# Performance work log

Hardware: AMD Instinct MI355X
Metric: run time of the kernel (lower is better)

## Reference

```python
import jax, jax.numpy as jnp
import numpy as np

# Dims: N tokens, D input, H expert hidden, O output, E experts, G gate hidden, K top-k
N, D, H, O, E, G, K = 8192, 1024, 2048, 1024, 8, 256, 2
BALANCE_COEF = 0.01


def setup_inputs() -> dict:
    key = jax.random.key(0)
    ks = jax.random.split(key, 12)
    def lin(k, shape, fan_in):
        return jax.random.normal(k, shape, jnp.float32) * (1.0 / np.sqrt(fan_in))
    return {
        "x":   jax.random.normal(ks[0], (N, D), jnp.float32),
        # gating MLP: D -> G -> E
        "Wg1": lin(ks[1], (D, G), D), "bg1": jnp.zeros((G,), jnp.float32),
        "Wg2": lin(ks[2], (G, E), G), "bg2": jnp.zeros((E,), jnp.float32),
        # stacked expert MLPs: D -> H -> H -> O (ExpertNetwork, num_layers=2)
        "W1": lin(ks[3], (E, D, H), D), "b1": jnp.zeros((E, H), jnp.float32),
        "W2": lin(ks[4], (E, H, H), H), "b2": jnp.zeros((E, H), jnp.float32),
        "W3": lin(ks[5], (E, H, O), H), "b3": jnp.zeros((E, O), jnp.float32),
    }


def reference(x, Wg1, bg1, Wg2, bg2, W1, b1, W2, b2, W3, b3):
    # Gating: 2-layer MLP -> softmax -> top-k -> renormalize (eval: no noise/dropout)
    logits = jnp.maximum(x @ Wg1 + bg1, 0.0) @ Wg2 + bg2            # [N, E]
    probs = jax.nn.softmax(logits, axis=-1)
    w, idx = jax.lax.top_k(probs, K)                                # [N, K]
    w = w / jnp.sum(w, axis=-1, keepdims=True)
    onehot = jax.nn.one_hot(idx, E, dtype=x.dtype)                  # [N, K, E]
    comb = jnp.sum(onehot * w[..., None], axis=1)                   # [N, E] per-token expert weight

    # Dense-equivalent combine: unselected tokens get weight 0, identical math to
    # the masked dispatch + scatter-add in the torch code.
    def expert_step(acc, params):
        W1e, b1e, W2e, b2e, W3e, b3e, we = params                   # we: [N]
        h = jnp.maximum(x @ W1e + b1e, 0.0)                         # [N, H]
        h = jnp.maximum(h @ W2e + b2e, 0.0)                         # [N, H]
        o = h @ W3e + b3e                                           # [N, O]
        return acc + o * we[:, None], None

    out, _ = jax.lax.scan(expert_step, jnp.zeros((N, O), x.dtype),
                          (W1, b1, W2, b2, W3, b3, comb.T))

    # aux losses: expert_usage[e] = sum_i mean_b(indices[b,i]==e)
    expert_usage = jnp.sum(onehot, axis=(0, 1)) / N                 # [E]
    balance_loss = jnp.mean((expert_usage - 1.0 / E) ** 2) * BALANCE_COEF
    return out, balance_loss, expert_usage
```

## Files before the change

### kernel.cpp

```cpp
#include <hip/hip_runtime.h>
#include <hip/hip_bf16.h>
#include <cstdint>
#include <cstddef>

#define N_TOK 8192
#define D_IN  1024
#define H_DIM 2048
#define O_DIM 1024
#define E_NUM 8
#define G_DIM 256
#define MAXTILES 136
#define MAXROWS  (MAXTILES*128)

typedef __attribute__((ext_vector_type(8))) __bf16 bf16x8;
typedef __attribute__((ext_vector_type(4))) __bf16 bf16x4;
typedef __attribute__((ext_vector_type(4))) float floatx4;

#define GCAST(p) ((__attribute__((address_space(1))) void*)(void*)(p))
#define LCAST(p) ((__attribute__((address_space(3))) void*)(p))

__global__ __launch_bounds__(256) void cast_x_kernel(const float* __restrict__ x,
                                                     __bf16* __restrict__ xb) {
  int i = (blockIdx.x * 256 + threadIdx.x) * 4;
  float4 v = *reinterpret_cast<const float4*>(x + i);
  bf16x4 o;
  o.x = (__bf16)v.x; o.y = (__bf16)v.y; o.z = (__bf16)v.z; o.w = (__bf16)v.w;
  *reinterpret_cast<bf16x4*>(xb + i) = o;
}

__global__ __launch_bounds__(256) void transpose_w_kernel(const float* __restrict__ src,
                                                          __bf16* __restrict__ dst,
                                                          int K, int N) {
  __shared__ float tl[32][33];
  int e = blockIdx.z;
  const float* s = src + (size_t)e * K * N;
  __bf16* d = dst + (size_t)e * K * N;
  int k0 = blockIdx.y * 32, n0 = blockIdx.x * 32;
  int t = threadIdx.x;
  int r = t >> 5, c = t & 31;
#pragma unroll
  for (int i = 0; i < 4; i++)
    tl[r + i * 8][c] = s[(size_t)(k0 + r + i * 8) * N + n0 + c];
  __syncthreads();
#pragma unroll
  for (int i = 0; i < 4; i++)
    d[(size_t)(n0 + r + i * 8) * K + k0 + c] = (__bf16)tl[c][r + i * 8];
}

__global__ __launch_bounds__(256) void gate1_kernel(const float* __restrict__ x,
                                                    const float* __restrict__ Wg1,
                                                    const float* __restrict__ bg1,
                                                    float* __restrict__ g) {
  __shared__ float As[32][68];
  __shared__ float Bs[32][68];
  int bn = blockIdx.x, bm = blockIdx.y;
  int t = threadIdx.x;
  int tm = t >> 4, tn = t & 15;
  float acc[4][4] = {};
  for (int k0 = 0; k0 < D_IN; k0 += 32) {
#pragma unroll
    for (int i = 0; i < 2; i++) {
      int idx = t + 256 * i;
      int row = idx >> 3, c4 = idx & 7;
      float4 v = *reinterpret_cast<const float4*>(
          x + (size_t)(bm * 64 + row) * D_IN + k0 + c4 * 4);
      As[c4 * 4 + 0][row] = v.x;
      As[c4 * 4 + 1][row] = v.y;
      As[c4 * 4 + 2][row] = v.z;
      As[c4 * 4 + 3][row] = v.w;
      int brow = idx >> 4, bc4 = idx & 15;
      float4 wv = *reinterpret_cast<const float4*>(
          Wg1 + (size_t)(k0 + brow) * G_DIM + bn * 64 + bc4 * 4);
      *reinterpret_cast<float4*>(&Bs[brow][bc4 * 4]) = wv;
    }
    __syncthreads();
#pragma unroll
    for (int k = 0; k < 32; k++) {
      float4 av = *reinterpret_cast<const float4*>(&As[k][tm * 4]);
      float4 bv = *reinterpret_cast<const float4*>(&Bs[k][tn * 4]);
      float a4[4] = {av.x, av.y, av.z, av.w};
      float b4[4] = {bv.x, bv.y, bv.z, bv.w};
#pragma unroll
      for (int r = 0; r < 4; r++)
#pragma unroll
        for (int c = 0; c < 4; c++) acc[r][c] = fmaf(a4[r], b4[c], acc[r][c]);
    }
    __syncthreads();
  }
  int gr = bm * 64 + tm * 4, gc = bn * 64 + tn * 4;
#pragma unroll
  for (int r = 0; r < 4; r++) {
    float4 o;
    o.x = fmaxf(acc[r][0] + bg1[gc + 0], 0.f);
    o.y = fmaxf(acc[r][1] + bg1[gc + 1], 0.f);
    o.z = fmaxf(acc[r][2] + bg1[gc + 2], 0.f);
    o.w = fmaxf(acc[r][3] + bg1[gc + 3], 0.f);
    *reinterpret_cast<float4*>(g + (size_t)(gr + r) * G_DIM + gc) = o;
  }
}

__global__ __launch_bounds__(256) void gate2_kernel(const float* __restrict__ g,
                                                    const float* __restrict__ Wg2,
                                                    const float* __restrict__ bg2,
                                                    int* __restrict__ top_idx,
                                                    float* __restrict__ top_w,
                                                    int* __restrict__ counts) {
  __shared__ float lg[32][9];
  int t = threadIdx.x;
  int tl = t >> 3, e = t & 7;
  int n = blockIdx.x * 32 + tl;
  const float* gr = g + (size_t)n * G_DIM;
  float acc = bg2[e];
  for (int i = 0; i < G_DIM; i += 4) {
    float4 v = *reinterpret_cast<const float4*>(gr + i);
    acc += v.x * Wg2[(i + 0) * E_NUM + e];
    acc += v.y * Wg2[(i + 1) * E_NUM + e];
    acc += v.z * Wg2[(i + 2) * E_NUM + e];
    acc += v.w * Wg2[(i + 3) * E_NUM + e];
  }
  lg[tl][e] = acc;
  __syncthreads();
  if (e == 0) {
    float l[8];
#pragma unroll
    for (int i = 0; i < 8; i++) l[i] = lg[tl][i];
    int i0 = 0;
    for (int i = 1; i < 8; i++)
      if (l[i] > l[i0]) i0 = i;
    int i1 = (i0 == 0) ? 1 : 0;
    for (int i = 0; i < 8; i++)
      if (i != i0 && l[i] > l[i1]) i1 = i;
    float d = expf(l[i1] - l[i0]);
    float w0 = 1.f / (1.f + d);
    float w1 = d * w0;
    top_idx[n * 2 + 0] = i0;
    top_idx[n * 2 + 1] = i1;
    top_w[n * 2 + 0] = w0;
    top_w[n * 2 + 1] = w1;
    atomicAdd(&counts[i0], 1);
    atomicAdd(&counts[i1], 1);
  }
}

__global__ void g3_kernel(const int* __restrict__ counts, int* __restrict__ cursors,
                          int* __restrict__ off_pad, int* __restrict__ ntiles,
                          int* __restrict__ tile_meta, float* __restrict__ out_tail) {
  if (threadIdx.x == 0) {
    int off = 0, nt = 0;
    float mse = 0.f;
    for (int e = 0; e < E_NUM; e++) {
      off_pad[e] = off;
      int c = counts[e];
      int tiles = (c + 127) >> 7;
      for (int i = 0; i < tiles; i++) {
        tile_meta[nt * 2 + 0] = e;
        tile_meta[nt * 2 + 1] = off + i * 128;
        nt++;
      }
      off += tiles << 7;
      cursors[e] = 0;
      float u = (float)c / (float)N_TOK;
      out_tail[1 + e] = u;
      float dd = u - 0.125f;
      mse += dd * dd;
    }
    *ntiles = nt;
    out_tail[0] = (mse / 8.0f) * 0.01f;
  }
}

__global__ __launch_bounds__(256) void init_rows_kernel(int* __restrict__ slot_token,
                                                        float* __restrict__ slot_w) {
  int s = blockIdx.x * 256 + threadIdx.x;
  slot_token[s] = 0;
  slot_w[s] = 0.f;
}

__global__ __launch_bounds__(256) void scatter_kernel(const int* __restrict__ top_idx,
                                                      const float* __restrict__ top_w,
                                                      const int* __restrict__ off_pad,
                                                      int* __restrict__ cursors,
                                                      int* __restrict__ slot_token,
                                                      float* __restrict__ slot_w) {
  int n = blockIdx.x * 256 + threadIdx.x;
#pragma unroll
  for (int k = 0; k < 2; k++) {
    int e = top_idx[n * 2 + k];
    int pos = atomicAdd(&cursors[e], 1);
    int s = off_pad[e] + pos;
    slot_token[s] = n;
    slot_w[s] = top_w[n * 2 + k];
  }
}

__global__ __launch_bounds__(256) void moe_gemm_kernel(
    const __bf16* __restrict__ A, int Astride, int gatherA,
    const __bf16* __restrict__ Wt, const float* __restrict__ bias,
    int Kdim, int Ndim,
    const int* __restrict__ tile_meta, const int* __restrict__ ntiles_p,
    const int* __restrict__ slot_token, const float* __restrict__ slot_w,
    __bf16* __restrict__ h_out, float* __restrict__ out_final, int finalMode) {
  int tile = blockIdx.y;
  if (tile >= *ntiles_p) return;
  __shared__ __bf16 As[128 * 32];
  __shared__ __bf16 Bs[128 * 32];
  int ex = tile_meta[tile * 2 + 0];
  int slot0 = tile_meta[tile * 2 + 1];
  int n0 = blockIdx.x * 128;
  int t = threadIdx.x, l = t & 63, w = t >> 6;

  size_t aoff[2], boff[2];
#pragma unroll
  for (int i = 0; i < 2; i++) {
    int gidx = (w * 2 + i) * 64 + l;
    int row = gidx >> 2, kch = gidx & 3;
    int sl = slot0 + row;
    long long rb = gatherA ? (long long)slot_token[sl] * Astride
                           : (long long)sl * Astride;
    aoff[i] = (size_t)rb + kch * 8;
    boff[i] = ((size_t)ex * Ndim + n0 + row) * (size_t)Kdim + kch * 8;
  }

  int wm = (w >> 1) * 64, wn = (w & 1) * 64;
  int lm = l & 15, lq = l >> 4;
  floatx4 acc[4][4] = {};

  for (int k0 = 0; k0 < Kdim; k0 += 32) {
#pragma unroll
    for (int i = 0; i < 2; i++) {
      __builtin_amdgcn_global_load_lds(GCAST(A + aoff[i] + k0),
                                       LCAST((char*)As + w * 2048 + i * 1024),
                                       16, 0, 0);
      __builtin_amdgcn_global_load_lds(GCAST(Wt + boff[i] + k0),
                                       LCAST((char*)Bs + w * 2048 + i * 1024),
                                       16, 0, 0);
    }
    __syncthreads();
    bf16x8 af[4], bfr[4];
#pragma unroll
    for (int i = 0; i < 4; i++)
      af[i] = *reinterpret_cast<const bf16x8*>(As + (wm + i * 16 + lm) * 32 + lq * 8);
#pragma unroll
    for (int j = 0; j < 4; j++)
      bfr[j] = *reinterpret_cast<const bf16x8*>(Bs + (wn + j * 16 + lm) * 32 + lq * 8);
#pragma unroll
    for (int i = 0; i < 4; i++)
#pragma unroll
      for (int j = 0; j < 4; j++)
        acc[i][j] = __builtin_amdgcn_mfma_f32_16x16x32_bf16(af[i], bfr[j], acc[i][j], 0, 0, 0);
    __syncthreads();
  }

  float bcol[4];
#pragma unroll
  for (int j = 0; j < 4; j++) bcol[j] = bias[(size_t)ex * Ndim + n0 + wn + j * 16 + lm];

  if (finalMode) {
#pragma unroll
    for (int i = 0; i < 4; i++) {
#pragma unroll
      for (int r = 0; r < 4; r++) {
        int sl = slot0 + wm + i * 16 + lq * 4 + r;
        int tok = slot_token[sl];
        float wgt = slot_w[sl];
        float* orow = out_final + (size_t)tok * Ndim + n0 + wn + lm;
#pragma unroll
        for (int j = 0; j < 4; j++) {
          float v = acc[i][j][r] + bcol[j];
          atomicAdd(orow + j * 16, wgt * v);
        }
      }
    }
  } else {
#pragma unroll
    for (int i = 0; i < 4; i++) {
#pragma unroll
      for (int r = 0; r < 4; r++) {
        int sl = slot0 + wm + i * 16 + lq * 4 + r;
        __bf16* hrow = h_out + (size_t)sl * Ndim + n0 + wn + lm;
#pragma unroll
        for (int j = 0; j < 4; j++) {
          float v = fmaxf(acc[i][j][r] + bcol[j], 0.f);
          hrow[j * 16] = (__bf16)v;
        }
      }
    }
  }
}

extern "C" void kernel_launch(void* const* d_in, const int* in_sizes, int n_in,
                              void* d_out, int out_size, void* d_ws, size_t ws_size,
                              hipStream_t stream) {
  const float* x   = (const float*)d_in[0];
  const float* Wg1 = (const float*)d_in[1];
  const float* bg1 = (const float*)d_in[2];
  const float* Wg2 = (const float*)d_in[3];
  const float* bg2 = (const float*)d_in[4];
  const float* W1  = (const float*)d_in[5];
  const float* b1  = (const float*)d_in[6];
  const float* W2  = (const float*)d_in[7];
  const float* b2  = (const float*)d_in[8];
  const float* W3  = (const float*)d_in[9];
  const float* b3  = (const float*)d_in[10];
  float* out = (float*)d_out;

  char* ws = (char*)d_ws;
  __bf16* x_bf       = (__bf16*)(ws + 0);
  __bf16* W1t        = (__bf16*)(ws + 16777216);
  __bf16* W2t        = (__bf16*)(ws + 50331648);
  __bf16* W3t        = (__bf16*)(ws + 117440512);
  __bf16* h1         = (__bf16*)(ws + 150994944);
  __bf16* h2         = (__bf16*)(ws + 222298112);
  float*  gbuf       = (float*) (ws + 293601280);
  int*    top_idx    = (int*)   (ws + 301989888);
  float*  top_w      = (float*) (ws + 302055424);
  int*    slot_token = (int*)   (ws + 302120960);
  float*  slot_w     = (float*) (ws + 302190592);
  int*    meta       = (int*)   (ws + 302260224);
  int* counts    = meta;
  int* cursors   = meta + 8;
  int* off_pad   = meta + 16;
  int* ntiles    = meta + 24;
  int* tile_meta = meta + 32;
  float* out_tail = out + (size_t)N_TOK * O_DIM;

  hipMemsetAsync(d_out, 0, ((size_t)N_TOK * O_DIM + 9) * sizeof(float), stream);
  hipMemsetAsync(meta, 0, 64, stream);

  cast_x_kernel<<<(N_TOK * D_IN) / 1024, 256, 0, stream>>>(x, x_bf);
  transpose_w_kernel<<<dim3(H_DIM / 32, D_IN / 32, E_NUM), 256, 0, stream>>>(W1, W1t, D_IN, H_DIM);
  transpose_w_kernel<<<dim3(H_DIM / 32, H_DIM / 32, E_NUM), 256, 0, stream>>>(W2, W2t, H_DIM, H_DIM);
  transpose_w_kernel<<<dim3(O_DIM / 32, H_DIM / 32, E_NUM), 256, 0, stream>>>(W3, W3t, H_DIM, O_DIM);

  gate1_kernel<<<dim3(G_DIM / 64, N_TOK / 64), 256, 0, stream>>>(x, Wg1, bg1, gbuf);
  gate2_kernel<<<N_TOK / 32, 256, 0, stream>>>(gbuf, Wg2, bg2, top_idx, top_w, counts);
  g3_kernel<<<1, 64, 0, stream>>>(counts, cursors, off_pad, ntiles, tile_meta, out_tail);
  init_rows_kernel<<<MAXROWS / 256, 256, 0, stream>>>(slot_token, slot_w);
  scatter_kernel<<<N_TOK / 256, 256, 0, stream>>>(top_idx, top_w, off_pad, cursors,
                                                  slot_token, slot_w);

  moe_gemm_kernel<<<dim3(H_DIM / 128, MAXTILES), 256, 0, stream>>>(
      x_bf, D_IN, 1, W1t, b1, D_IN, H_DIM, tile_meta, ntiles, slot_token, slot_w,
      h1, nullptr, 0);
  moe_gemm_kernel<<<dim3(H_DIM / 128, MAXTILES), 256, 0, stream>>>(
      h1, H_DIM, 0, W2t, b2, H_DIM, H_DIM, tile_meta, ntiles, slot_token, slot_w,
      h2, nullptr, 0);
  moe_gemm_kernel<<<dim3(O_DIM / 128, MAXTILES), 256, 0, stream>>>(
      h2, H_DIM, 0, W3t, b3, H_DIM, O_DIM, tile_meta, ntiles, slot_token, slot_w,
      nullptr, out, 1);
}
```

Measured before the change: 1.148 ms.

## Swizzle GEMM LDS tiles, widen weight transpose, fuse slot init, skip padded atomics

Applies an XOR swizzle to the k-chunk placement in the MoE GEMM's LDS tiles so the MFMA fragment reads hit fewer bank conflicts. Rewrites the weight transpose to use 64x64 tiles with float4 loads and 16-byte bf16 stores. Folds the slot_token/slot_w zeroing into g3_kernel, which removes one launch but does the zeroing in a single block. Also skips the output atomicAdds for padded rows whose weight is zero.

```diff
diff --git a/kernel.cpp b/kernel.cpp
--- a/kernel.cpp
+++ b/kernel.cpp
@@ -31,20 +31,28 @@
 __global__ __launch_bounds__(256) void transpose_w_kernel(const float* __restrict__ src,
                                                           __bf16* __restrict__ dst,
                                                           int K, int N) {
-  __shared__ float tl[32][33];
+  __shared__ float tl[64][68];
   int e = blockIdx.z;
   const float* s = src + (size_t)e * K * N;
   __bf16* d = dst + (size_t)e * K * N;
-  int k0 = blockIdx.y * 32, n0 = blockIdx.x * 32;
+  int k0 = blockIdx.y * 64, n0 = blockIdx.x * 64;
   int t = threadIdx.x;
-  int r = t >> 5, c = t & 31;
-#pragma unroll
-  for (int i = 0; i < 4; i++)
-    tl[r + i * 8][c] = s[(size_t)(k0 + r + i * 8) * N + n0 + c];
+  int kr = t >> 4, nc = t & 15;
+#pragma unroll
+  for (int p = 0; p < 4; p++) {
+    float4 v = *reinterpret_cast<const float4*>(
+        s + (size_t)(k0 + kr + p * 16) * N + n0 + nc * 4);
+    *reinterpret_cast<float4*>(&tl[kr + p * 16][nc * 4]) = v;
+  }
   __syncthreads();
-#pragma unroll
-  for (int i = 0; i < 4; i++)
-    d[(size_t)(n0 + r + i * 8) * K + k0 + c] = (__bf16)tl[c][r + i * 8];
+  int n = t >> 2, kg = t & 3;
+#pragma unroll
+  for (int p = 0; p < 2; p++) {
+    bf16x8 o;
+#pragma unroll
+    for (int j = 0; j < 8; j++) o[j] = (__bf16)tl[p * 32 + kg * 8 + j][n];
+    *reinterpret_cast<bf16x8*>(d + (size_t)(n0 + n) * K + k0 + p * 32 + kg * 8) = o;
+  }
 }
 
 __global__ __launch_bounds__(256) void gate1_kernel(const float* __restrict__ x,
@@ -144,7 +152,8 @@
 
 __global__ void g3_kernel(const int* __restrict__ counts, int* __restrict__ cursors,
                           int* __restrict__ off_pad, int* __restrict__ ntiles,
-                          int* __restrict__ tile_meta, float* __restrict__ out_tail) {
+                          int* __restrict__ tile_meta, float* __restrict__ out_tail,
+                          int* __restrict__ slot_token, float* __restrict__ slot_w) {
   if (threadIdx.x == 0) {
     int off = 0, nt = 0;
     float mse = 0.f;
@@ -167,13 +176,10 @@
     *ntiles = nt;
     out_tail[0] = (mse / 8.0f) * 0.01f;
   }
-}
-
-__global__ __launch_bounds__(256) void init_rows_kernel(int* __restrict__ slot_token,
-                                                        float* __restrict__ slot_w) {
-  int s = blockIdx.x * 256 + threadIdx.x;
-  slot_token[s] = 0;
-  slot_w[s] = 0.f;
+  for (int s = threadIdx.x; s < MAXROWS; s += 256) {
+    slot_token[s] = 0;
+    slot_w[s] = 0.f;
+  }
 }
 
 __global__ __launch_bounds__(256) void scatter_kernel(const int* __restrict__ top_idx,
@@ -213,7 +219,8 @@
 #pragma unroll
   for (int i = 0; i < 2; i++) {
     int gidx = (w * 2 + i) * 64 + l;
-    int row = gidx >> 2, kch = gidx & 3;
+    int row = gidx >> 2;
+    int kch = (gidx & 3) ^ ((row >> 1) & 3);
     int sl = slot0 + row;
     long long rb = gatherA ? (long long)slot_token[sl] * Astride
                            : (long long)sl * Astride;
@@ -238,11 +245,17 @@
     __syncthreads();
     bf16x8 af[4], bfr[4];
 #pragma unroll
-    for (int i = 0; i < 4; i++)
-      af[i] = *reinterpret_cast<const bf16x8*>(As + (wm + i * 16 + lm) * 32 + lq * 8);
-#pragma unroll
-    for (int j = 0; j < 4; j++)
-      bfr[j] = *reinterpret_cast<const bf16x8*>(Bs + (wn + j * 16 + lm) * 32 + lq * 8);
+    for (int i = 0; i < 4; i++) {
+      int r = wm + i * 16 + lm;
+      int s = lq ^ ((r >> 1) & 3);
+      af[i] = *reinterpret_cast<const bf16x8*>(As + r * 32 + s * 8);
+    }
+#pragma unroll
+    for (int j = 0; j < 4; j++) {
+      int r = wn + j * 16 + lm;
+      int s = lq ^ ((r >> 1) & 3);
+      bfr[j] = *reinterpret_cast<const bf16x8*>(Bs + r * 32 + s * 8);
+    }
 #pragma unroll
     for (int i = 0; i < 4; i++)
 #pragma unroll
@@ -263,11 +276,13 @@
         int sl = slot0 + wm + i * 16 + lq * 4 + r;
         int tok = slot_token[sl];
         float wgt = slot_w[sl];
-        float* orow = out_final + (size_t)tok * Ndim + n0 + wn + lm;
-#pragma unroll
-        for (int j = 0; j < 4; j++) {
-          float v = acc[i][j][r] + bcol[j];
-          atomicAdd(orow + j * 16, wgt * v);
+        if (wgt != 0.f) {
+          float* orow = out_final + (size_t)tok * Ndim + n0 + wn + lm;
+#pragma unroll
+          for (int j = 0; j < 4; j++) {
+            float v = acc[i][j][r] + bcol[j];
+            atomicAdd(orow + j * 16, wgt * v);
+          }
         }
       }
     }
@@ -328,14 +343,14 @@
   hipMemsetAsync(meta, 0, 64, stream);
 
   cast_x_kernel<<<(N_TOK * D_IN) / 1024, 256, 0, stream>>>(x, x_bf);
-  transpose_w_kernel<<<dim3(H_DIM / 32, D_IN / 32, E_NUM), 256, 0, stream>>>(W1, W1t, D_IN, H_DIM);
-  transpose_w_kernel<<<dim3(H_DIM / 32, H_DIM / 32, E_NUM), 256, 0, stream>>>(W2, W2t, H_DIM, H_DIM);
-  transpose_w_kernel<<<dim3(O_DIM / 32, H_DIM / 32, E_NUM), 256, 0, stream>>>(W3, W3t, H_DIM, O_DIM);
+  transpose_w_kernel<<<dim3(H_DIM / 64, D_IN / 64, E_NUM), 256, 0, stream>>>(W1, W1t, D_IN, H_DIM);
+  transpose_w_kernel<<<dim3(H_DIM / 64, H_DIM / 64, E_NUM), 256, 0, stream>>>(W2, W2t, H_DIM, H_DIM);
+  transpose_w_kernel<<<dim3(O_DIM / 64, H_DIM / 64, E_NUM), 256, 0, stream>>>(W3, W3t, H_DIM, O_DIM);
 
   gate1_kernel<<<dim3(G_DIM / 64, N_TOK / 64), 256, 0, stream>>>(x, Wg1, bg1, gbuf);
   gate2_kernel<<<N_TOK / 32, 256, 0, stream>>>(gbuf, Wg2, bg2, top_idx, top_w, counts);
-  g3_kernel<<<1, 64, 0, stream>>>(counts, cursors, off_pad, ntiles, tile_meta, out_tail);
-  init_rows_kernel<<<MAXROWS / 256, 256, 0, stream>>>(slot_token, slot_w);
+  g3_kernel<<<1, 256, 0, stream>>>(counts, cursors, off_pad, ntiles, tile_meta, out_tail,
+                                   slot_token, slot_w);
   scatter_kernel<<<N_TOK / 256, 256, 0, stream>>>(top_idx, top_w, off_pad, cursors,
                                                   slot_token, slot_w);
 
```

After: 1.095 ms. 4.6% less time.
